# Kernel tuning notes

Measured on AMD Instinct MI355X. Metric: run time of the kernel, lower is better.

The kernel has to match this reference:

```python
import jax, jax.numpy as jnp
import numpy as np

ANGLE_THR = float(np.pi / 2.0)
N_PTS = 3072
# nuScenes per-class anchor sizes (l, w, h) hard-coded in FrustumClusterProposer.__init__
ANCHORS = np.array([[4.63, 1.97, 1.74], [6.93, 2.51, 2.84], [6.37, 2.85, 3.19],
                    [10.5, 2.94, 3.47], [12.29, 2.9, 3.87], [0.5, 2.53, 0.98],
                    [2.11, 0.77, 1.47], [1.7, 0.6, 1.28], [0.73, 0.67, 1.77],
                    [0.41, 0.41, 1.07]], dtype=np.float32)


def setup_inputs() -> dict:
    key = jax.random.key(0)
    k1, k2 = jax.random.split(key)
    pts = jax.random.normal(k1, (N_PTS, 3), jnp.float32) * 15.0  # metric-scale frustum points
    lbl = jax.random.randint(k2, (N_PTS,), 0, 10)                # per-point 2D-detector class id
    return {"frust_points": pts, "frust_labels": lbl, "anchors": jnp.asarray(ANCHORS)}


def _cluster(points, labels_cls, anchors, angle_thr=ANGLE_THR):
    """Faithful port of CombinedAngleClusterer.__call__ (greedy angle/dist clustering + merge)."""
    n = points.shape[0]
    f32 = points.dtype
    pos = jnp.arange(n)

    # curr_anchor_max_diffs: xy replaced by max(l, w) per class
    xy_max = anchors[:, :2].max(axis=1)
    amd = jnp.stack([xy_max, xy_max, anchors[:, 2]], axis=1)  # [10, 3]
    anchor_r2 = jnp.linalg.norm(anchors, axis=1) / 2.0        # [10]

    # pairwise displacements, distances and calc_angles matrix (vectorized over rows)
    diff = points[None, :, :] - points[:, None, :]            # [n, n, 3]
    dists = jnp.linalg.norm(diff, axis=-1)                    # cdist
    dot = -jnp.einsum('id,ijd->ij', points, diff)             # l1 = -p_i, l2 = p_j - p_i
    denom = jnp.linalg.norm(points, axis=1)[:, None] * dists + 1e-8
    angles = jnp.arccos(jnp.clip(dot / denom, -1.0, 1.0))     # clip for numerical safety

    dl0 = jnp.full((n,), -1, jnp.int32).at[0].set(0)          # dist_labels
    cc0 = jnp.full((n,), -1, jnp.int32)                       # cluster_classes

    def step(carry, _):
        dl, cc, cur, lab = carry
        cls_cur = labels_cls[cur]
        cc = cc.at[lab].set(jnp.where(cc[lab] < 0, cls_cur, cc[lab]))
        nv = dl == -1                                          # not visited
        cm = dl == lab                                         # current cluster
        cmf = cm.astype(f32)
        centre = (points * cmf[:, None]).sum(0) / cmf.sum()
        drow = dists[cur]
        dmin = jnp.min(jnp.where(nv, drow, jnp.inf))
        dmax = jnp.max(jnp.where(nv, drow, -jnp.inf))
        dcost = (drow - dmin) / (dmax - dmin + 1e-8)           # norm01 over unvisited
        lcost = jnp.minimum(jnp.abs(labels_cls - cls_cur).astype(f32), 1.0)
        ci = jnp.argmin(jnp.where(nv, dcost + lcost, jnp.inf))
        d = points[cur] - points[ci]
        new_c = (jnp.any(jnp.abs(d) > amd[cls_cur])
                 | (jnp.max(jnp.where(cm, angles[cur], -jnp.inf)) < angle_thr)
                 | (labels_cls[ci] != cls_cur)
                 | (jnp.linalg.norm(d) > anchor_r2[cls_cur])
                 | (jnp.linalg.norm(centre - points[ci]) > anchor_r2[cls_cur]))
        lab = lab + new_c.astype(jnp.int32)
        dl = dl.at[ci].set(lab)
        return (dl, cc, ci, lab), None

    (dl, cc, _, _), _ = jax.lax.scan(step, (dl0, cc0, jnp.int32(0), jnp.int32(0)), None, length=n - 1)

    # cluster statistics (padded to n clusters; num_clusters = max label, EXCLUSIVE, as in torch)
    counts = jax.ops.segment_sum(jnp.ones((n,), jnp.int32), dl, num_segments=n)
    centres = jax.ops.segment_sum(points, dl, num_segments=n) / jnp.maximum(counts, 1).astype(f32)[:, None]
    num_clusters = dl.max()
    order = jnp.argsort(-jnp.where(pos < num_clusters, counts, -1))
    ocls = cc[order]
    ocentres = centres[order]

    def merge(carry, i):
        keep, dl = carry
        idx = order[i]
        active = (i < num_clusters) & keep[i]
        r2 = anchor_r2[cc[idx]]
        cond = (active & (pos > i) & (pos < num_clusters) & keep
                & (ocls == cc[idx])
                & (jnp.linalg.norm(ocentres - centres[idx], axis=1) < r2))
        keep = keep & ~cond
        merged = jnp.zeros((n,), bool).at[order].set(cond)     # order-position -> cluster-id
        dl = jnp.where(merged[dl], idx, dl)
        return (keep, dl), None

    (_, dl), _ = jax.lax.scan(merge, (jnp.ones((n,), bool), dl), pos)
    return dl


def reference(frust_points, frust_labels, anchors):
    return _cluster(frust_points, frust_labels.astype(jnp.int32), anchors)
```

## Files before the change

kernel.cpp:

```cpp
#include <hip/hip_runtime.h>
#include <math.h>

#define NPTS 3072
#define BLK  256
#define NW   4
#define NSL  8
#define NKB  48
#define NCLS 10

#pragma clang fp contract(off)

__device__ __forceinline__ unsigned umin32(unsigned a, unsigned b) { return a < b ? a : b; }

__device__ __forceinline__ unsigned rowmin4_u32(unsigned x) {
    unsigned t;
    t = (unsigned)__builtin_amdgcn_update_dpp(-1, (int)x, 0x111, 0xF, 0xF, false); x = x < t ? x : t;
    t = (unsigned)__builtin_amdgcn_update_dpp(-1, (int)x, 0x112, 0xF, 0xF, false); x = x < t ? x : t;
    t = (unsigned)__builtin_amdgcn_update_dpp(-1, (int)x, 0x114, 0xF, 0xF, false); x = x < t ? x : t;
    t = (unsigned)__builtin_amdgcn_update_dpp(-1, (int)x, 0x118, 0xF, 0xF, false); x = x < t ? x : t;
    return x;
}

__device__ __forceinline__ unsigned wavemin_u32(unsigned x) {
    unsigned r = rowmin4_u32(x);
    unsigned a = (unsigned)__builtin_amdgcn_readlane((int)r, 15);
    unsigned b = (unsigned)__builtin_amdgcn_readlane((int)r, 31);
    unsigned c = (unsigned)__builtin_amdgcn_readlane((int)r, 47);
    unsigned d = (unsigned)__builtin_amdgcn_readlane((int)r, 63);
    return umin32(umin32(a, b), umin32(c, d));
}

__device__ __forceinline__ float readlanef(float v, int l) {
    return __int_as_float(__builtin_amdgcn_readlane(__float_as_int(v), l));
}

template<int NS>
__device__ __forceinline__ void sweep_step(const float (&sxr)[NSL], const float (&syr)[NSL],
                                           const float (&szr)[NSL], const unsigned (&mmr)[NSL],
                                           float pcx, float pcy, float pcz,
                                           unsigned &kbest, unsigned &mbest,
                                           float &bx, float &by, float &bz)
{
    float ss[NS];
    #pragma unroll
    for (int i = 0; i < NS; ++i) {
        float dx = pcx - sxr[i], dy = pcy - syr[i], dz = pcz - szr[i];
        ss[i] = (dx*dx + dy*dy) + dz*dz;
    }
    float m;
    if constexpr (NS == 5)
        m = fminf(fminf(fminf(ss[0], ss[1]), fminf(ss[2], ss[3])), ss[4]);
    else if constexpr (NS == 6)
        m = fminf(fminf(fminf(ss[0], ss[1]), fminf(ss[2], ss[3])), fminf(ss[4], ss[5]));
    else
        m = fminf(fminf(fminf(ss[0], ss[1]), fminf(ss[2], ss[3])),
                  fminf(fminf(ss[4], ss[5]), fminf(ss[6], ss[7])));
    kbest = __float_as_uint(m);
    unsigned mb = 0xFFFFFFFFu;
    #pragma unroll
    for (int i = 0; i < NS; ++i) {
        unsigned ci = (ss[i] == m) ? mmr[i] : 0xFFFFFFFFu;
        mb = umin32(mb, ci);
    }
    mbest = mb;
    bx = sxr[0]; by = syr[0]; bz = szr[0];
    #pragma unroll
    for (int i = 1; i < NS; ++i) {
        bool w = (mmr[i] == mb);
        bx = w ? sxr[i] : bx; by = w ? syr[i] : by; bz = w ? szr[i] : bz;
    }
}

template<int NS>
__device__ __forceinline__ void poison_step(float (&sxr)[NSL], const unsigned (&mmr)[NSL],
                                            unsigned wm)
{
    #pragma unroll
    for (int i = 0; i < NS; ++i)
        if (mmr[i] == wm) sxr[i] = 3e19f;
}

#define WALK_INNER(NS)                                                          \
    _Pragma("unroll 4")                                                         \
    for (int k = 0; k < iters; ++k) {                                           \
        unsigned kbest, mbest; float bx, by, bz;                                \
        sweep_step<NS>(sxr, syr, szr, mmr, pcx, pcy, pcz, kbest, mbest, bx, by, bz); \
        unsigned wk = wavemin_u32(kbest);                                       \
        bool cand = (kbest == wk);                                              \
        unsigned long long msk = __ballot(cand);                                \
        if (msk & (msk - 1)) {                     \
            unsigned wm2 = wavemin_u32(cand ? mbest : 0xFFFFFFFFu);             \
            msk = __ballot(cand && (mbest == wm2));                             \
        }                                                                       \
        int wl = __ffsll((unsigned long long)msk) - 1;                          \
        unsigned wm = (unsigned)__builtin_amdgcn_readlane((int)mbest, wl);      \
        float pix = readlanef(bx, wl), piy = readlanef(by, wl), piz = readlanef(bz, wl); \
        pos = (int)(wm & 0xFFFu);                                               \
        poison_step<NS>(sxr, mmr, wm);                                          \
        *((lane == 0) ? &recM16[u] : &sdump[lane]) = (unsigned short)pos;       \
        pcx = pix; pcy = piy; pcz = piz;                                        \
        ++u;                                                                    \
    }

__global__ __launch_bounds__(BLK)
void frustum_cluster(const float* __restrict__ pts,
                     const int* __restrict__ lblg,
                     const float* __restrict__ anch,
                     int* __restrict__ out,
                     int* __restrict__ ws)
{
    const int tid  = threadIdx.x;
    const int lane = tid & 63;
    const int wid  = tid >> 6;

    int*    dlg    = ws + 16;
    float4* gstats = (float4*)(ws + 8192);

    __shared__ float4 gpts[NPTS];
    __shared__ unsigned short recM16[NPTS];
    __shared__ unsigned short startv[NPTS];
    __shared__ unsigned short sdump[64];
    __shared__ unsigned short walkS16[65];
    __shared__ unsigned short walkCls16[16];
    __shared__ float amdxy[NCLS], amdz[NCLS];
    __shared__ unsigned vthr[NCLS], wthr[NCLS];
    __shared__ int cntL[NCLS], curL[NCLS], baseL[NCLS];
    __shared__ int cntC[NCLS], curC[NCLS], baseC[NCLS];
    __shared__ int cntW[16], baseW[16];
    __shared__ int p0s, nclusS;

    if (tid < NCLS) {
        float l = anch[tid*3+0], w = anch[tid*3+1], h = anch[tid*3+2];
        amdxy[tid] = fmaxf(l, w);
        amdz[tid]  = h;
        float r2 = sqrtf((l*l + w*w) + h*h) * 0.5f;
        unsigned lo = 0u, hi = 0x7F7FFFFFu;
        while (hi - lo > 1u) {
            unsigned mid = lo + ((hi - lo) >> 1);
            if (sqrtf(__uint_as_float(mid)) <= r2) lo = mid; else hi = mid;
        }
        vthr[tid] = lo;
        lo = 0u; hi = 0x7F7FFFFFu;
        while (hi - lo > 1u) {
            unsigned mid = lo + ((hi - lo) >> 1);
            if (sqrtf(__uint_as_float(mid)) < r2) lo = mid; else hi = mid;
        }
        wthr[tid] = lo;
        cntL[tid] = 0; curL[tid] = 0; cntC[tid] = 0; curC[tid] = 0;
    }
    if (tid < 65) walkS16[tid] = (unsigned short)NPTS;
    if (tid < 16) { walkCls16[tid] = 0; cntW[tid] = 0; }
    __syncthreads();
    for (int j = tid; j < NPTS; j += BLK) atomicAdd(&cntL[lblg[j]], 1);
    __syncthreads();
    if (tid == 0) { int acc = 0; for (int c = 0; c < NCLS; ++c) { baseL[c] = acc; acc += cntL[c]; } }
    __syncthreads();
    for (int j = tid; j < NPTS; j += BLK) {
        int c = lblg[j];
        int pos = baseL[c] + atomicAdd(&curL[c], 1);
        float4 e;
        e.x = pts[3*j]; e.y = pts[3*j+1]; e.z = pts[3*j+2];
        e.w = __uint_as_float(((unsigned)j << 16) | ((unsigned)c << 12) | (unsigned)pos);
        gpts[pos] = e;
        if (j == 0) p0s = pos;
    }
    __syncthreads();

    if (wid == 0) {
        int baseLn = 0, cntLn = 0;
        if (lane < NCLS) { baseLn = baseL[lane]; cntLn = cntL[lane]; }
        const int p0 = p0s;
        int pos = p0;
        int cls = lblg[0];
        unsigned walked = 1u << cls;
        float sxr[NSL], syr[NSL], szr[NSL];
        unsigned mmr[NSL];
        float pcx = pts[0], pcy = pts[1], pcz = pts[2];
        int u = 1;
        if (lane == 0) recM16[0] = (unsigned short)p0;

        for (int wix = 0; wix < NCLS; ++wix) {
            if (lane == 0) {
                walkS16[wix]   = (unsigned short)(u - 1);
                walkCls16[wix] = (unsigned short)cls;
            }
            int base_c = __builtin_amdgcn_readlane(baseLn, cls);
            int cnt_c  = __builtin_amdgcn_readlane(cntLn, cls);
            #pragma unroll
            for (int i = 0; i < NSL; ++i) {
                int off = lane + (i << 6);
                int p = base_c + off;
                bool in = off < cnt_c;
                float4 e = gpts[in ? p : 0];
                bool v = in && (p != pos);
                sxr[i] = v ? e.x : 3e19f;
                syr[i] = v ? e.y : 0.f;
                szr[i] = v ? e.z : 0.f;
                mmr[i] = in ? __float_as_uint(e.w) : 0xFFFFFFFFu;
            }
            int nsC = (cnt_c + 63) >> 6;
            int iters = cnt_c - 1;

            if (nsC <= 5)      { WALK_INNER(5) }
            else if (nsC == 6) { WALK_INNER(6) }
            else               { WALK_INNER(8) }

            if (u >= NPTS) break;

            {
                unsigned kbest = 0xFFFFFFFFu, mbest = 0xFFFFFFFFu;
                float bx = 0.f, by = 0.f, bz = 0.f;
                for (int k2 = 0; k2 < NKB; ++k2) {
                    int p = lane + (k2 << 6);
                    float4 e = gpts[p];
                    unsigned meta = __float_as_uint(e.w);
                    float dx = pcx - e.x, dy = pcy - e.y, dz = pcz - e.z;
                    float s = (dx*dx + dy*dy) + dz*dz;
                    unsigned key = __float_as_uint(s);
                    bool ok = !((walked >> ((meta >> 12) & 15u)) & 1u);
                    if (ok && (key < kbest || (key == kbest && meta < mbest))) {
                        kbest = key; mbest = meta; bx = e.x; by = e.y; bz = e.z;
                    }
                }
                unsigned wk = wavemin_u32(kbest);
                bool cand = (kbest == wk);
                unsigned wm = wavemin_u32(cand ? mbest : 0xFFFFFFFFu);
                unsigned long long msk = __ballot(cand && (mbest == wm));
                int wl = __ffsll((unsigned long long)msk) - 1;
                float pix = readlanef(bx, wl), piy = readlanef(by, wl), piz = readlanef(bz, wl);
                pos = (int)(wm & 0xFFFu);
                cls = (int)((wm >> 12) & 15u);
                walked |= 1u << cls;
                *((lane == 0) ? &recM16[u] : &sdump[lane]) = (unsigned short)pos;
                pcx = pix; pcy = piy; pcz = piz;
                ++u;
            }
        }
    }
    __syncthreads();

    if (wid == 0) {
        int w = lane;
        int sW = (int)walkS16[w];
        int eW = (int)walkS16[w + 1];
        bool exists = sW < NPTS;
        int cls = (int)walkCls16[exists ? w : 0];
        float axy = amdxy[cls], az = amdz[cls];
        unsigned Vc = vthr[cls];
        int pos0 = (int)recM16[exists ? sW : 0];
        float4 pe = gpts[pos0];
        float prevx = pe.x, prevy = pe.y, prevz = pe.z;
        float sx = prevx, sy = prevy, sz = prevz, scnt = 1.0f;
        int cnt = 1;
        if (exists) startv[sW] = (unsigned short)sW;
        int u = sW + 1;
        int posn = (int)recM16[(exists && u < eW) ? u : 0];
        for (;;) {
            unsigned long long alive = __ballot(u < eW);
            if (!alive) break;
            bool act = (u < eW);
            float4 ec = gpts[act ? posn : 0];
            int posn2 = (int)recM16[(u + 1 < eW) ? (u + 1) : 0];
            float pix = ec.x, piy = ec.y, piz = ec.z;
            float dx = prevx - pix, dy = prevy - piy, dz = prevz - piz;
            float seS = (dx*dx + dy*dy) + dz*dz;
            bool a1 = (fabsf(dx) > axy) | (fabsf(dy) > axy) | (fabsf(dz) > az);
            float icx = sx / scnt, icy = sy / scnt, icz = sz / scnt;
            float ex = icx - pix, ey = icy - piy, ez = icz - piz;
            float seC = (ex*ex + ey*ey) + ez*ez;
            bool nc = a1 | (__float_as_uint(seS) > Vc) | (__float_as_uint(seC) > Vc);
            if (act & nc) startv[sW + cnt] = (unsigned short)u;
            cnt += (act & nc) ? 1 : 0;
            scnt = nc ? 1.0f : (scnt + 1.0f);
            sx = nc ? pix : (sx + pix);
            sy = nc ? piy : (sy + piy);
            sz = nc ? piz : (sz + piz);
            prevx = pix; prevy = piy; prevz = piz;
            posn = posn2;
            ++u;
        }
        if (exists) cntW[w] = cnt;
    }
    __syncthreads();

    if (tid == 0) {
        int acc = 0;
        for (int c = 0; c < NCLS; ++c) { baseW[c] = acc; acc += cntW[c]; }
        nclusS = acc - 1;
    }
    __syncthreads();

    if (wid == 0) {
        for (int w2 = 0; w2 < NCLS; ++w2) {
            int sW = (int)walkS16[w2];
            if (sW >= NPTS) break;
            int bW = baseW[w2], cW = cntW[w2];
            if (bW == sW) continue;
            for (int j = lane; j < cW; j += 64) {
                unsigned short v = startv[sW + j];
                startv[bW + j] = v;
            }
        }
    }
    __syncthreads();
    const int nclus = nclusS;

    for (int c2 = tid; c2 <= nclus; c2 += BLK) {
        int s0 = startv[c2];
        int s1e = (c2 < nclus) ? (int)startv[c2+1] : NPTS;
        float ax = 0.f, ay = 0.f, az = 0.f;
        int clsF = 0;
        for (int s = s0; s < s1e; ++s) {
            float4 e = gpts[recM16[s]];
            unsigned pk = __float_as_uint(e.w);
            if (s == s0) clsF = (int)((pk >> 12) & 15u);
            ax = ax + e.x; ay = ay + e.y; az = az + e.z;
            dlg[pk >> 16] = c2;
        }
        if (c2 < nclus) {
            float fc = (float)(s1e - s0);
            float4 g;
            g.x = ax / fc; g.y = ay / fc; g.z = az / fc;
            g.w = __uint_as_float(((unsigned)(s1e - s0) << 4) | (unsigned)clsF);
            gstats[c2] = g;
        }
    }
    __syncthreads();

    for (int c2 = tid; c2 < nclus; c2 += BLK)
        atomicAdd(&cntC[__float_as_uint(gstats[c2].w) & 15u], 1);
    __syncthreads();
    if (tid == 0) { int acc = 0; for (int c = 0; c < NCLS; ++c) { baseC[c] = acc; acc += cntC[c]; } }
    __syncthreads();

    for (int c2 = tid; c2 < nclus; c2 += BLK) {
        unsigned gw = __float_as_uint(gstats[c2].w);
        int cl = (int)(gw & 15u);
        int slot = baseC[cl] + atomicAdd(&curC[cl], 1);
        recM16[slot] = (unsigned short)(gw >> 4);
        startv[slot] = (unsigned short)c2;
    }
    __syncthreads();

    for (int slot = tid; slot < nclus; slot += BLK) {
        int cl = 0;
        #pragma unroll
        for (int q = 1; q < NCLS; ++q) cl += (int)(slot >= baseC[q]);
        int b0 = baseC[cl], b1 = b0 + cntC[cl];
        int cnt = (int)recM16[slot], id = (int)startv[slot];
        int r = 0;
        for (int s2 = b0; s2 < b1; ++s2) {
            int cnt2 = (int)recM16[s2], id2 = (int)startv[s2];
            r += (int)((cnt2 > cnt) || (cnt2 == cnt && id2 < id));
        }
        float4 g = gstats[id];
        float4 oe;
        oe.x = g.x; oe.y = g.y; oe.z = g.z;
        oe.w = __uint_as_float(((unsigned)id << 1) | 1u);
        gpts[b0 + r] = oe;
    }
    __syncthreads();

    unsigned short* remap16 = startv;
    for (int c2 = tid; c2 < NPTS; c2 += BLK) remap16[c2] = (unsigned short)c2;
    __syncthreads();

    for (int cl = wid; cl < NCLS; cl += NW) {
        int b0 = baseC[cl], b1 = b0 + cntC[cl];
        unsigned Wc = wthr[cl];
        for (int i = b0; i < b1; ++i) {
            float4 ei = gpts[i];
            unsigned wi = __float_as_uint(ei.w);
            if (wi & 1u) {
                int orgI = (int)(wi >> 1);
                for (int j = i + 1 + lane; j < b1; j += 64) {
                    float4 ej = gpts[j];
                    unsigned wj = __float_as_uint(ej.w);
                    if (wj & 1u) {
                        float ddx = ej.x - ei.x, ddy = ej.y - ei.y, ddz = ej.z - ei.z;
                        float sdd = (ddx*ddx + ddy*ddy) + ddz*ddz;
                        if (__float_as_uint(sdd) <= Wc) {
                            gpts[j].w = __uint_as_float(wj & ~1u);
                            remap16[wj >> 1] = (unsigned short)orgI;
                        }
                    }
                }
            }
        }
    }
    __syncthreads();

    for (int p = tid; p < NPTS; p += BLK) out[p] = (int)remap16[dlg[p]];
}

extern "C" void kernel_launch(void* const* d_in, const int* in_sizes, int n_in,
                              void* d_out, int out_size, void* d_ws, size_t ws_size,
                              hipStream_t stream) {
    const float* pts  = (const float*)d_in[0];
    const int*   lbl  = (const int*)d_in[1];
    const float* anch = (const float*)d_in[2];
    frustum_cluster<<<dim3(1), dim3(BLK), 0, stream>>>(pts, lbl, anch,
                                                       (int*)d_out, (int*)d_ws);
}
```

Measured before the change: 1.808 ms.

## Precompute per-point 4-nearest same-class neighbours to shortcut the greedy walk

After: 3.481 ms. 1.93x slower.

```diff
diff --git a/kernel.cpp b/kernel.cpp
--- a/kernel.cpp
+++ b/kernel.cpp
@@ -72,33 +72,79 @@
 }
 
 template<int NS>
-__device__ __forceinline__ void poison_step(float (&sxr)[NSL], const unsigned (&mmr)[NSL],
-                                            unsigned wm)
+__device__ __forceinline__ void poison_pos(float (&sxr)[NSL], const unsigned (&mmr)[NSL],
+                                           unsigned wpos)
 {
     #pragma unroll
     for (int i = 0; i < NS; ++i)
-        if (mmr[i] == wm) sxr[i] = 3e19f;
+        if ((mmr[i] & 0xFFFu) == wpos) sxr[i] = 3e19f;
+}
+
+__device__ __forceinline__ bool nn_unv(int e, int base_c,
+        unsigned long long vb0, unsigned long long vb1, unsigned long long vb2,
+        unsigned long long vb3, unsigned long long vb4, unsigned long long vb5,
+        unsigned long long vb6, unsigned long long vb7)
+{
+    int ix = e - base_c;
+    int w = ix >> 6;
+    unsigned long long vw = w==0?vb0 : w==1?vb1 : w==2?vb2 : w==3?vb3
+                          : w==4?vb4 : w==5?vb5 : w==6?vb6 : vb7;
+    return (e != 0xFFF) && !((vw >> (ix & 63)) & 1ull);
+}
+__device__ __forceinline__ void nn_setv(int ix,
+        unsigned long long &vb0, unsigned long long &vb1, unsigned long long &vb2,
+        unsigned long long &vb3, unsigned long long &vb4, unsigned long long &vb5,
+        unsigned long long &vb6, unsigned long long &vb7)
+{
+    unsigned long long bit = 1ull << (ix & 63);
+    int w = ix >> 6;
+    vb0 = (w==0) ? (vb0|bit) : vb0;
+    vb1 = (w==1) ? (vb1|bit) : vb1;
+    vb2 = (w==2) ? (vb2|bit) : vb2;
+    vb3 = (w==3) ? (vb3|bit) : vb3;
+    vb4 = (w==4) ? (vb4|bit) : vb4;
+    vb5 = (w==5) ? (vb5|bit) : vb5;
+    vb6 = (w==6) ? (vb6|bit) : vb6;
+    vb7 = (w==7) ? (vb7|bit) : vb7;
 }
 
 #define WALK_INNER(NS)                                                          \
-    _Pragma("unroll 4")                                                         \
     for (int k = 0; k < iters; ++k) {                                           \
-        unsigned kbest, mbest; float bx, by, bz;                                \
-        sweep_step<NS>(sxr, syr, szr, mmr, pcx, pcy, pcz, kbest, mbest, bx, by, bz); \
-        unsigned wk = wavemin_u32(kbest);                                       \
-        bool cand = (kbest == wk);                                              \
-        unsigned long long msk = __ballot(cand);                                \
-        if (msk & (msk - 1)) {                     \
-            unsigned wm2 = wavemin_u32(cand ? mbest : 0xFFFFFFFFu);             \
-            msk = __ballot(cand && (mbest == wm2));                             \
+        int nxt = -1;                                                           \
+        if (iters - k > 4) {               \
+            unsigned long long lst = knn4[pos];        \
+            unsigned llo = (unsigned)__builtin_amdgcn_readfirstlane((int)(unsigned)lst);         \
+            unsigned lhi = (unsigned)__builtin_amdgcn_readfirstlane((int)(unsigned)(lst >> 32)); \
+            int e0 = (int)(llo & 0xFFFFu), e1 = (int)(llo >> 16);               \
+            int e2 = (int)(lhi & 0xFFFFu), e3 = (int)(lhi >> 16);               \
+            bool u0 = nn_unv(e0, base_c, vb0,vb1,vb2,vb3,vb4,vb5,vb6,vb7);      \
+            bool u1 = nn_unv(e1, base_c, vb0,vb1,vb2,vb3,vb4,vb5,vb6,vb7);      \
+            bool u2 = nn_unv(e2, base_c, vb0,vb1,vb2,vb3,vb4,vb5,vb6,vb7);      \
+            bool u3 = nn_unv(e3, base_c, vb0,vb1,vb2,vb3,vb4,vb5,vb6,vb7);      \
+            nxt = u0 ? e0 : u1 ? e1 : u2 ? e2 : u3 ? e3 : -1;                   \
         }                                                                       \
-        int wl = __ffsll((unsigned long long)msk) - 1;                          \
-        unsigned wm = (unsigned)__builtin_amdgcn_readlane((int)mbest, wl);      \
-        float pix = readlanef(bx, wl), piy = readlanef(by, wl), piz = readlanef(bz, wl); \
-        pos = (int)(wm & 0xFFFu);                                               \
-        poison_step<NS>(sxr, mmr, wm);                                          \
+        if (nxt >= 0) {                                                \
+            pos = nxt;                                                          \
+            float4 wp = gpts[pos];          \
+            pcx = wp.x; pcy = wp.y; pcz = wp.z;                                 \
+        } else {                                           \
+            unsigned kbest, mbest; float bx, by, bz;                            \
+            sweep_step<NS>(sxr, syr, szr, mmr, pcx, pcy, pcz, kbest, mbest, bx, by, bz); \
+            unsigned wk = wavemin_u32(kbest);                                   \
+            bool cand = (kbest == wk);                                          \
+            unsigned long long msk = __ballot(cand);                            \
+            if (msk & (msk - 1)) {                    \
+                unsigned wm2 = wavemin_u32(cand ? mbest : 0xFFFFFFFFu);         \
+                msk = __ballot(cand && (mbest == wm2));                         \
+            }                                                                   \
+            int wl = __ffsll((unsigned long long)msk) - 1;                      \
+            unsigned wm = (unsigned)__builtin_amdgcn_readlane((int)mbest, wl);  \
+            pos = (int)(wm & 0xFFFu);                                           \
+            pcx = readlanef(bx, wl); pcy = readlanef(by, wl); pcz = readlanef(bz, wl); \
+        }                                                                       \
+        poison_pos<NS>(sxr, mmr, (unsigned)pos);                                \
+        nn_setv(pos - base_c, vb0,vb1,vb2,vb3,vb4,vb5,vb6,vb7);                 \
         *((lane == 0) ? &recM16[u] : &sdump[lane]) = (unsigned short)pos;       \
-        pcx = pix; pcy = piy; pcz = piz;                                        \
         ++u;                                                                    \
     }
 
@@ -117,6 +163,7 @@
     float4* gstats = (float4*)(ws + 8192);
 
     __shared__ float4 gpts[NPTS];
+    __shared__ unsigned long long knn4[NPTS];
     __shared__ unsigned short recM16[NPTS];
     __shared__ unsigned short startv[NPTS];
     __shared__ unsigned short sdump[64];
@@ -166,6 +213,35 @@
     }
     __syncthreads();
 
+    for (int r = 0; r < NPTS / BLK; ++r) {
+        int p = tid + (r << 8);
+        float4 ep = gpts[p];
+        unsigned mp = __float_as_uint(ep.w);
+        int pcls = (int)((mp >> 12) & 15u);
+        int b = baseL[pcls], cnt = cntL[pcls];
+        unsigned k0=~0u,k1=~0u,k2=~0u,k3=~0u, m0=~0u,m1=~0u,m2=~0u,m3=~0u;
+        for (int j = 0; j < cnt; ++j) {
+            int q = b + j;
+            float4 eq = gpts[q];
+            float dx = ep.x - eq.x, dy = ep.y - eq.y, dz = ep.z - eq.z;
+            float ssq = (dx*dx + dy*dy) + dz*dz;
+            unsigned kk = (q == p) ? 0xFFFFFFFFu : __float_as_uint(ssq);
+            unsigned mm = __float_as_uint(eq.w);
+            bool l3 = (kk<k3)|((kk==k3)&(mm<m3)); k3=l3?kk:k3; m3=l3?mm:m3;
+            bool s2 = (k3<k2)|((k3==k2)&(m3<m2));
+            unsigned tk=k2, tm=m2; k2=s2?k3:k2; m2=s2?m3:m2; k3=s2?tk:k3; m3=s2?tm:m3;
+            bool s1 = (k2<k1)|((k2==k1)&(m2<m1));
+            tk=k1; tm=m1; k1=s1?k2:k1; m1=s1?m2:m1; k2=s1?tk:k2; m2=s1?tm:m2;
+            bool s0 = (k1<k0)|((k1==k0)&(m1<m0));
+            tk=k0; tm=m0; k0=s0?k1:k0; m0=s0?m1:m0; k1=s0?tk:k1; m1=s0?tm:m1;
+        }
+        knn4[p] =  (unsigned long long)(m0 & 0xFFFu)
+                | ((unsigned long long)(m1 & 0xFFFu) << 16)
+                | ((unsigned long long)(m2 & 0xFFFu) << 32)
+                | ((unsigned long long)(m3 & 0xFFFu) << 48);
+    }
+    __syncthreads();
+
     if (wid == 0) {
         int baseLn = 0, cntLn = 0;
         if (lane < NCLS) { baseLn = baseL[lane]; cntLn = cntL[lane]; }
@@ -176,6 +252,7 @@
         float sxr[NSL], syr[NSL], szr[NSL];
         unsigned mmr[NSL];
         float pcx = pts[0], pcy = pts[1], pcz = pts[2];
+        unsigned long long vb0=0,vb1=0,vb2=0,vb3=0,vb4=0,vb5=0,vb6=0,vb7=0;
         int u = 1;
         if (lane == 0) recM16[0] = (unsigned short)p0;
 
@@ -198,6 +275,8 @@
                 szr[i] = v ? e.z : 0.f;
                 mmr[i] = in ? __float_as_uint(e.w) : 0xFFFFFFFFu;
             }
+            vb0=0; vb1=0; vb2=0; vb3=0; vb4=0; vb5=0; vb6=0; vb7=0;
+            nn_setv(pos - base_c, vb0,vb1,vb2,vb3,vb4,vb5,vb6,vb7);
             int nsC = (cnt_c + 63) >> 6;
             int iters = cnt_c - 1;
 
@@ -224,9 +303,13 @@
                 }
                 unsigned wk = wavemin_u32(kbest);
                 bool cand = (kbest == wk);
-                unsigned wm = wavemin_u32(cand ? mbest : 0xFFFFFFFFu);
-                unsigned long long msk = __ballot(cand && (mbest == wm));
+                unsigned long long msk = __ballot(cand);
+                if (msk & (msk - 1)) {
+                    unsigned wm2 = wavemin_u32(cand ? mbest : 0xFFFFFFFFu);
+                    msk = __ballot(cand && (mbest == wm2));
+                }
                 int wl = __ffsll((unsigned long long)msk) - 1;
+                unsigned wm = (unsigned)__builtin_amdgcn_readlane((int)mbest, wl);
                 float pix = readlanef(bx, wl), piy = readlanef(by, wl), piz = readlanef(bz, wl);
                 pos = (int)(wm & 0xFFFu);
                 cls = (int)((wm >> 12) & 15u);
```
